# Optimization experiments

Hardware: AMD Instinct MI355X
Metric: run time of the kernel (lower is better)

Reference implementation:

```python
import jax, jax.numpy as jnp
import numpy as np

B, E, O, H = 4096, 1024, 16, 1024  # batch, embed_dim, num_ops, hidden_dim


def setup_inputs() -> dict:
    key = jax.random.key(0)
    k1, k2, k3, k4, k5, k6 = jax.random.split(key, 6)
    s1 = 1.0 / np.sqrt(E)
    s2 = 1.0 / np.sqrt(H)
    return {
        "x_aug": jax.random.normal(k1, (B, E), dtype=jnp.float32),
        "op_idx": jax.random.randint(k2, (B,), 0, O, dtype=jnp.int32),
        "W1": jax.random.normal(k3, (E, O, H), dtype=jnp.float32) * s1,  # DenseGeneral kernel: embed -> (ops, hidden)
        "b1": jnp.zeros((O, H), dtype=jnp.float32),
        "W2": jax.random.normal(k4, (H, O, H), dtype=jnp.float32) * s2,  # per-op second layer (diagonal of DenseGeneral)
        "b2": jnp.zeros((O, H), dtype=jnp.float32),
    }


def reference(x_aug, op_idx, W1, b1, W2, b2):
    # h1[b,o,h] = relu(sum_e x[b,e] W1[e,o,h] + b1[o,h])
    h1 = jax.nn.relu(jnp.einsum("be,eoh->boh", x_aug, W1) + b1)
    # h2[b,o,g] = relu(sum_h h1[b,o,h] W2[h,o,g] + b2[o,g])  (per-op MLP)
    h2 = jax.nn.relu(jnp.einsum("boh,hog->bog", h1, W2) + b2)
    # select the chosen operator's output per example
    idx = jnp.broadcast_to(op_idx[:, None, None], (x_aug.shape[0], 1, h2.shape[-1]))
    return jnp.take_along_axis(h2, idx, axis=1).squeeze(1)  # [B, H]
```

## Files before the change

### kernel.cpp

```cpp
#include <hip/hip_runtime.h>

#define Bn 4096
#define En 1024
#define On 16
#define Hn 1024
#define OHn (On * Hn)

#define BM 64
#define BN 128
#define BK 64

using floatx4 = __attribute__((ext_vector_type(4))) float;
using float4v = __attribute__((ext_vector_type(4))) float;
using bf16x8  = __attribute__((ext_vector_type(8))) __bf16;
using short8v = __attribute__((ext_vector_type(8))) short;

__device__ inline unsigned short f2bf(float f) {
    unsigned u = __builtin_bit_cast(unsigned, f);
    u += 0x7fffu + ((u >> 16) & 1u);
    return (unsigned short)(u >> 16);
}

__global__ void bucket_kernel(const int* __restrict__ op_idx,
                              int* __restrict__ sorted_idx,
                              int* __restrict__ offsets) {
    __shared__ int cnt[On], cur[On], off[On + 1];
    int tid = threadIdx.x;
    if (tid < On) { cnt[tid] = 0; cur[tid] = 0; }
    __syncthreads();
    for (int i = tid; i < Bn; i += blockDim.x) atomicAdd(&cnt[op_idx[i]], 1);
    __syncthreads();
    if (tid == 0) {
        int s = 0;
        for (int o = 0; o < On; ++o) { off[o] = s; s += cnt[o]; }
        off[On] = s;
    }
    __syncthreads();
    for (int i = tid; i < Bn; i += blockDim.x) {
        int o = op_idx[i];
        int p = off[o] + atomicAdd(&cur[o], 1);
        sorted_idx[p] = i;
    }
    if (tid <= On) offsets[tid] = off[tid];
}

__global__ __launch_bounds__(256) void gemm1_kernel(
    const float* __restrict__ x, const float* __restrict__ W1,
    const float* __restrict__ bias1, const int* __restrict__ sorted_idx,
    const int* __restrict__ offsets, unsigned short* __restrict__ h1) {
    int o = blockIdx.z;
    int off = offsets[o];
    int cnt = offsets[o + 1] - off;
    int m0 = blockIdx.y * BM;
    if (m0 >= cnt) return;
    int n0 = blockIdx.x * BN;

    __shared__ unsigned short As[8][BM][8];
    __shared__ unsigned short Bs[8][BN][8];

    int tid = threadIdx.x;

    int arow = tid & 63;
    int ag = tid >> 6;
    const float* aptr = nullptr;
    if (m0 + arow < cnt) aptr = x + (size_t)sorted_idx[off + m0 + arow] * En;

    int bn = tid & 127;
    int bg0 = (tid >> 7) * 4;
    const float* bptr = W1 + (size_t)o * Hn + n0 + bn;

    float a_pre[16] = {};
    float b_pre[32];

    floatx4 acc[2][4] = {};
    int lane = tid & 63;
    int wave = tid >> 6;
    int wm = (wave >> 1) * 32;
    int wn = (wave & 1) * 64;
    int l15 = lane & 15;
    int kg = lane >> 4;

#pragma unroll
    for (int i = 0; i < 2; ++i) {
        int k = (ag + 4 * i) * 8;
        if (aptr) {
            *(float4v*)&a_pre[i * 8]     = *(const float4v*)(aptr + k);
            *(float4v*)&a_pre[i * 8 + 4] = *(const float4v*)(aptr + k + 4);
        }
    }
#pragma unroll
    for (int g = 0; g < 4; ++g)
#pragma unroll
        for (int j = 0; j < 8; ++j)
            b_pre[g * 8 + j] = bptr[(size_t)((bg0 + g) * 8 + j) * OHn];

    for (int kt = 0; kt < En; kt += BK) {
#pragma unroll
        for (int i = 0; i < 2; ++i) {
            short8v v;
#pragma unroll
            for (int j = 0; j < 8; ++j) v[j] = (short)f2bf(a_pre[i * 8 + j]);
            *(short8v*)&As[ag + 4 * i][arow][0] = v;
        }
#pragma unroll
        for (int g = 0; g < 4; ++g) {
            short8v v;
#pragma unroll
            for (int j = 0; j < 8; ++j) v[j] = (short)f2bf(b_pre[g * 8 + j]);
            *(short8v*)&Bs[bg0 + g][bn][0] = v;
        }
        __syncthreads();

        int ktn = kt + BK;
        if (ktn < En) {
#pragma unroll
            for (int i = 0; i < 2; ++i) {
                int k = ktn + (ag + 4 * i) * 8;
                if (aptr) {
                    *(float4v*)&a_pre[i * 8]     = *(const float4v*)(aptr + k);
                    *(float4v*)&a_pre[i * 8 + 4] = *(const float4v*)(aptr + k + 4);
                }
            }
#pragma unroll
            for (int g = 0; g < 4; ++g)
#pragma unroll
                for (int j = 0; j < 8; ++j)
                    b_pre[g * 8 + j] = bptr[(size_t)(ktn + (bg0 + g) * 8 + j) * OHn];
        }

#pragma unroll
        for (int ks = 0; ks < 2; ++ks) {
            int g = ks * 4 + kg;
            bf16x8 af[2], bfr[4];
#pragma unroll
            for (int mt = 0; mt < 2; ++mt) af[mt] = *(const bf16x8*)&As[g][wm + mt * 16 + l15][0];
#pragma unroll
            for (int nt = 0; nt < 4; ++nt) bfr[nt] = *(const bf16x8*)&Bs[g][wn + nt * 16 + l15][0];
#pragma unroll
            for (int mt = 0; mt < 2; ++mt)
#pragma unroll
                for (int nt = 0; nt < 4; ++nt)
                    acc[mt][nt] = __builtin_amdgcn_mfma_f32_16x16x32_bf16(af[mt], bfr[nt], acc[mt][nt], 0, 0, 0);
        }
        __syncthreads();
    }

    int r4 = (lane >> 4) * 4;
#pragma unroll
    for (int nt = 0; nt < 4; ++nt) {
        int col = n0 + wn + nt * 16 + l15;
        float bv = bias1[o * Hn + col];
#pragma unroll
        for (int mt = 0; mt < 2; ++mt) {
#pragma unroll
            for (int r = 0; r < 4; ++r) {
                int row = m0 + wm + mt * 16 + r4 + r;
                if (row < cnt) {
                    float v = acc[mt][nt][r] + bv;
                    v = v > 0.f ? v : 0.f;
                    h1[(size_t)(off + row) * Hn + col] = f2bf(v);
                }
            }
        }
    }
}

__global__ __launch_bounds__(256) void gemm2_kernel(
    const unsigned short* __restrict__ h1, const float* __restrict__ W2,
    const float* __restrict__ bias2, const int* __restrict__ sorted_idx,
    const int* __restrict__ offsets, float* __restrict__ out) {
    int o = blockIdx.z;
    int off = offsets[o];
    int cnt = offsets[o + 1] - off;
    int m0 = blockIdx.y * BM;
    if (m0 >= cnt) return;
    int n0 = blockIdx.x * BN;

    __shared__ unsigned short As[8][BM][8];
    __shared__ unsigned short Bs[8][BN][8];

    int tid = threadIdx.x;

    int arow = tid & 63;
    int ag = tid >> 6;
    const unsigned short* aptr = nullptr;
    if (m0 + arow < cnt) aptr = h1 + (size_t)(off + m0 + arow) * Hn;

    int bn = tid & 127;
    int bg0 = (tid >> 7) * 4;
    const float* bptr = W2 + (size_t)o * Hn + n0 + bn;

    short8v a_pre[2] = {};
    float b_pre[32];

    floatx4 acc[2][4] = {};
    int lane = tid & 63;
    int wave = tid >> 6;
    int wm = (wave >> 1) * 32;
    int wn = (wave & 1) * 64;
    int l15 = lane & 15;
    int kg = lane >> 4;

#pragma unroll
    for (int i = 0; i < 2; ++i)
        if (aptr) a_pre[i] = *(const short8v*)(aptr + (ag + 4 * i) * 8);
#pragma unroll
    for (int g = 0; g < 4; ++g)
#pragma unroll
        for (int j = 0; j < 8; ++j)
            b_pre[g * 8 + j] = bptr[(size_t)((bg0 + g) * 8 + j) * OHn];

    for (int kt = 0; kt < Hn; kt += BK) {
#pragma unroll
        for (int i = 0; i < 2; ++i)
            *(short8v*)&As[ag + 4 * i][arow][0] = a_pre[i];
#pragma unroll
        for (int g = 0; g < 4; ++g) {
            short8v v;
#pragma unroll
            for (int j = 0; j < 8; ++j) v[j] = (short)f2bf(b_pre[g * 8 + j]);
            *(short8v*)&Bs[bg0 + g][bn][0] = v;
        }
        __syncthreads();

        int ktn = kt + BK;
        if (ktn < Hn) {
#pragma unroll
            for (int i = 0; i < 2; ++i)
                if (aptr) a_pre[i] = *(const short8v*)(aptr + ktn + (ag + 4 * i) * 8);
#pragma unroll
            for (int g = 0; g < 4; ++g)
#pragma unroll
                for (int j = 0; j < 8; ++j)
                    b_pre[g * 8 + j] = bptr[(size_t)(ktn + (bg0 + g) * 8 + j) * OHn];
        }

#pragma unroll
        for (int ks = 0; ks < 2; ++ks) {
            int g = ks * 4 + kg;
            bf16x8 af[2], bfr[4];
#pragma unroll
            for (int mt = 0; mt < 2; ++mt) af[mt] = *(const bf16x8*)&As[g][wm + mt * 16 + l15][0];
#pragma unroll
            for (int nt = 0; nt < 4; ++nt) bfr[nt] = *(const bf16x8*)&Bs[g][wn + nt * 16 + l15][0];
#pragma unroll
            for (int mt = 0; mt < 2; ++mt)
#pragma unroll
                for (int nt = 0; nt < 4; ++nt)
                    acc[mt][nt] = __builtin_amdgcn_mfma_f32_16x16x32_bf16(af[mt], bfr[nt], acc[mt][nt], 0, 0, 0);
        }
        __syncthreads();
    }

    int r4 = (lane >> 4) * 4;
    float bv[4];
#pragma unroll
    for (int nt = 0; nt < 4; ++nt) bv[nt] = bias2[o * Hn + n0 + wn + nt * 16 + l15];
#pragma unroll
    for (int mt = 0; mt < 2; ++mt) {
#pragma unroll
        for (int r = 0; r < 4; ++r) {
            int row = m0 + wm + mt * 16 + r4 + r;
            if (row < cnt) {
                int b = sorted_idx[off + row];
                float* orow = out + (size_t)b * Hn + n0 + wn + l15;
#pragma unroll
                for (int nt = 0; nt < 4; ++nt) {
                    float v = acc[mt][nt][r] + bv[nt];
                    orow[nt * 16] = v > 0.f ? v : 0.f;
                }
            }
        }
    }
}

extern "C" void kernel_launch(void* const* d_in, const int* in_sizes, int n_in,
                              void* d_out, int out_size, void* d_ws, size_t ws_size,
                              hipStream_t stream) {
    const float* x      = (const float*)d_in[0];
    const int*   op_idx = (const int*)d_in[1];
    const float* W1     = (const float*)d_in[2];
    const float* bias1  = (const float*)d_in[3];
    const float* W2     = (const float*)d_in[4];
    const float* bias2  = (const float*)d_in[5];
    float* out = (float*)d_out;

    char* ws = (char*)d_ws;
    int* offsets    = (int*)ws;
    int* sorted_idx = (int*)(ws + 256);
    unsigned short* h1 = (unsigned short*)(ws + 256 + 16384);

    hipLaunchKernelGGL(bucket_kernel, dim3(1), dim3(1024), 0, stream,
                       op_idx, sorted_idx, offsets);
    dim3 grid(Hn / BN, Bn / BM, On);
    hipLaunchKernelGGL(gemm1_kernel, grid, dim3(256), 0, stream,
                       x, W1, bias1, sorted_idx, offsets, h1);
    hipLaunchKernelGGL(gemm2_kernel, grid, dim3(256), 0, stream,
                       h1, W2, bias2, sorted_idx, offsets, out);
}
```

Baseline: 263.0 us.

## Pre-transpose weights and pre-gather x to bf16, load tiles via global_load_lds

```diff
diff --git a/kernel.cpp b/kernel.cpp
--- a/kernel.cpp
+++ b/kernel.cpp
@@ -4,7 +4,6 @@
 #define En 1024
 #define On 16
 #define Hn 1024
-#define OHn (On * Hn)
 
 #define BM 64
 #define BN 128
@@ -13,6 +12,7 @@
 using floatx4 = __attribute__((ext_vector_type(4))) float;
 using float4v = __attribute__((ext_vector_type(4))) float;
 using bf16x8  = __attribute__((ext_vector_type(8))) __bf16;
+using short4v = __attribute__((ext_vector_type(4))) short;
 using short8v = __attribute__((ext_vector_type(8))) short;
 
 __device__ inline unsigned short f2bf(float f) {
@@ -20,6 +20,10 @@
     u += 0x7fffu + ((u >> 16) & 1u);
     return (unsigned short)(u >> 16);
 }
+
+#define GLOAD16(gp, lp) __builtin_amdgcn_global_load_lds( \
+    (const __attribute__((address_space(1))) unsigned int*)(gp), \
+    (__attribute__((address_space(3))) unsigned int*)(lp), 16, 0, 0)
 
 __global__ void bucket_kernel(const int* __restrict__ op_idx,
                               int* __restrict__ sorted_idx,
@@ -44,13 +48,46 @@
     if (tid <= On) offsets[tid] = off[tid];
 }
 
+__global__ __launch_bounds__(256) void wtrans_kernel(const float* __restrict__ W,
+                                                     unsigned short* __restrict__ Wt) {
+    __shared__ float tile[64][65];
+    int o = blockIdx.z, e0 = blockIdx.y * 64, h0 = blockIdx.x * 64;
+    int t = threadIdx.x;
+    int er = t >> 4, c4 = (t & 15) * 4;
+#pragma unroll
+    for (int r = 0; r < 4; ++r) {
+        const float* p = W + ((size_t)(e0 + er + 16 * r) * On + o) * Hn + h0 + c4;
+        *(float4v*)&tile[er + 16 * r][c4] = *(const float4v*)p;
+    }
+    __syncthreads();
+    int hr = t >> 3, e8 = (t & 7) * 8;
+#pragma unroll
+    for (int r = 0; r < 2; ++r) {
+        short8v v;
+#pragma unroll
+        for (int j = 0; j < 8; ++j) v[j] = (short)f2bf(tile[e8 + j][hr + 32 * r]);
+        *(short8v*)(Wt + ((size_t)o * Hn + (h0 + hr + 32 * r)) * En + e0 + e8) = v;
+    }
+}
+
+__global__ __launch_bounds__(256) void xprep_kernel(const float* __restrict__ x,
+                                                    const int* __restrict__ sorted_idx,
+                                                    unsigned short* __restrict__ xs) {
+    int row = blockIdx.x;
+    int src = sorted_idx[row];
+    int t = threadIdx.x;
+    float4v f = *(const float4v*)(x + (size_t)src * En + t * 4);
+    short4v v = { (short)f2bf(f[0]), (short)f2bf(f[1]),
+                  (short)f2bf(f[2]), (short)f2bf(f[3]) };
+    *(short4v*)(xs + (size_t)row * En + t * 4) = v;
+}
+
 __global__ __launch_bounds__(256) void gemm1_kernel(
-    const float* __restrict__ x, const float* __restrict__ W1,
-    const float* __restrict__ bias1, const int* __restrict__ sorted_idx,
-    const int* __restrict__ offsets, unsigned short* __restrict__ h1) {
+    const unsigned short* __restrict__ xs, const unsigned short* __restrict__ Wt,
+    const float* __restrict__ bias1, const int* __restrict__ offsets,
+    unsigned short* __restrict__ h1) {
     int o = blockIdx.z;
-    int off = offsets[o];
-    int cnt = offsets[o + 1] - off;
+    int off = offsets[o], cnt = offsets[o + 1] - off;
     int m0 = blockIdx.y * BM;
     if (m0 >= cnt) return;
     int n0 = blockIdx.x * BN;
@@ -58,76 +95,28 @@
     __shared__ unsigned short As[8][BM][8];
     __shared__ unsigned short Bs[8][BN][8];
 
-    int tid = threadIdx.x;
-
-    int arow = tid & 63;
-    int ag = tid >> 6;
-    const float* aptr = nullptr;
-    if (m0 + arow < cnt) aptr = x + (size_t)sorted_idx[off + m0 + arow] * En;
-
-    int bn = tid & 127;
-    int bg0 = (tid >> 7) * 4;
-    const float* bptr = W1 + (size_t)o * Hn + n0 + bn;
-
-    float a_pre[16] = {};
-    float b_pre[32];
+    int tid = threadIdx.x, lane = tid & 63, wave = tid >> 6;
+    const unsigned short* Abase = xs + (size_t)(off + m0) * En;
+    const unsigned short* Bbase = Wt + ((size_t)o * Hn + n0) * En;
 
     floatx4 acc[2][4] = {};
-    int lane = tid & 63;
-    int wave = tid >> 6;
-    int wm = (wave >> 1) * 32;
-    int wn = (wave & 1) * 64;
-    int l15 = lane & 15;
-    int kg = lane >> 4;
-
-#pragma unroll
-    for (int i = 0; i < 2; ++i) {
-        int k = (ag + 4 * i) * 8;
-        if (aptr) {
-            *(float4v*)&a_pre[i * 8]     = *(const float4v*)(aptr + k);
-            *(float4v*)&a_pre[i * 8 + 4] = *(const float4v*)(aptr + k + 4);
-        }
-    }
-#pragma unroll
-    for (int g = 0; g < 4; ++g)
-#pragma unroll
-        for (int j = 0; j < 8; ++j)
-            b_pre[g * 8 + j] = bptr[(size_t)((bg0 + g) * 8 + j) * OHn];
+    int wm = (wave >> 1) * 32, wn = (wave & 1) * 64;
+    int l15 = lane & 15, kg = lane >> 4;
 
     for (int kt = 0; kt < En; kt += BK) {
 #pragma unroll
         for (int i = 0; i < 2; ++i) {
-            short8v v;
-#pragma unroll
-            for (int j = 0; j < 8; ++j) v[j] = (short)f2bf(a_pre[i * 8 + j]);
-            *(short8v*)&As[ag + 4 * i][arow][0] = v;
-        }
-#pragma unroll
-        for (int g = 0; g < 4; ++g) {
-            short8v v;
-#pragma unroll
-            for (int j = 0; j < 8; ++j) v[j] = (short)f2bf(b_pre[g * 8 + j]);
-            *(short8v*)&Bs[bg0 + g][bn][0] = v;
-        }
-        __syncthreads();
-
-        int ktn = kt + BK;
-        if (ktn < En) {
-#pragma unroll
-            for (int i = 0; i < 2; ++i) {
-                int k = ktn + (ag + 4 * i) * 8;
-                if (aptr) {
-                    *(float4v*)&a_pre[i * 8]     = *(const float4v*)(aptr + k);
-                    *(float4v*)&a_pre[i * 8 + 4] = *(const float4v*)(aptr + k + 4);
-                }
-            }
-#pragma unroll
-            for (int g = 0; g < 4; ++g)
-#pragma unroll
-                for (int j = 0; j < 8; ++j)
-                    b_pre[g * 8 + j] = bptr[(size_t)(ktn + (bg0 + g) * 8 + j) * OHn];
-        }
-
+            int g = wave * 2 + i;
+            GLOAD16(Abase + (size_t)lane * En + kt + g * 8, &As[g][0][0]);
+        }
+#pragma unroll
+        for (int i = 0; i < 4; ++i) {
+            int idx = wave * 4 + i;
+            int g = idx >> 1, half = idx & 1;
+            GLOAD16(Bbase + (size_t)(half * 64 + lane) * En + kt + g * 8,
+                    &Bs[g][half * 64][0]);
+        }
+        __syncthreads();
 #pragma unroll
         for (int ks = 0; ks < 2; ++ks) {
             int g = ks * 4 + kg;
@@ -166,12 +155,11 @@
 }
 
 __global__ __launch_bounds__(256) void gemm2_kernel(
-    const unsigned short* __restrict__ h1, const float* __restrict__ W2,
+    const unsigned short* __restrict__ h1, const unsigned short* __restrict__ Wt,
     const float* __restrict__ bias2, const int* __restrict__ sorted_idx,
     const int* __restrict__ offsets, float* __restrict__ out) {
     int o = blockIdx.z;
-    int off = offsets[o];
-    int cnt = offsets[o + 1] - off;
+    int off = offsets[o], cnt = offsets[o + 1] - off;
     int m0 = blockIdx.y * BM;
     if (m0 >= cnt) return;
     int n0 = blockIdx.x * BN;
@@ -179,62 +167,28 @@
     __shared__ unsigned short As[8][BM][8];
     __shared__ unsigned short Bs[8][BN][8];
 
-    int tid = threadIdx.x;
-
-    int arow = tid & 63;
-    int ag = tid >> 6;
-    const unsigned short* aptr = nullptr;
-    if (m0 + arow < cnt) aptr = h1 + (size_t)(off + m0 + arow) * Hn;
-
-    int bn = tid & 127;
-    int bg0 = (tid >> 7) * 4;
-    const float* bptr = W2 + (size_t)o * Hn + n0 + bn;
-
-    short8v a_pre[2] = {};
-    float b_pre[32];
+    int tid = threadIdx.x, lane = tid & 63, wave = tid >> 6;
+    const unsigned short* Abase = h1 + (size_t)(off + m0) * Hn;
+    const unsigned short* Bbase = Wt + ((size_t)o * Hn + n0) * Hn;
 
     floatx4 acc[2][4] = {};
-    int lane = tid & 63;
-    int wave = tid >> 6;
-    int wm = (wave >> 1) * 32;
-    int wn = (wave & 1) * 64;
-    int l15 = lane & 15;
-    int kg = lane >> 4;
-
-#pragma unroll
-    for (int i = 0; i < 2; ++i)
-        if (aptr) a_pre[i] = *(const short8v*)(aptr + (ag + 4 * i) * 8);
-#pragma unroll
-    for (int g = 0; g < 4; ++g)
-#pragma unroll
-        for (int j = 0; j < 8; ++j)
-            b_pre[g * 8 + j] = bptr[(size_t)((bg0 + g) * 8 + j) * OHn];
+    int wm = (wave >> 1) * 32, wn = (wave & 1) * 64;
+    int l15 = lane & 15, kg = lane >> 4;
 
     for (int kt = 0; kt < Hn; kt += BK) {
 #pragma unroll
-        for (int i = 0; i < 2; ++i)
-            *(short8v*)&As[ag + 4 * i][arow][0] = a_pre[i];
-#pragma unroll
-        for (int g = 0; g < 4; ++g) {
-            short8v v;
-#pragma unroll
-            for (int j = 0; j < 8; ++j) v[j] = (short)f2bf(b_pre[g * 8 + j]);
-            *(short8v*)&Bs[bg0 + g][bn][0] = v;
-        }
-        __syncthreads();
-
-        int ktn = kt + BK;
-        if (ktn < Hn) {
-#pragma unroll
-            for (int i = 0; i < 2; ++i)
-                if (aptr) a_pre[i] = *(const short8v*)(aptr + ktn + (ag + 4 * i) * 8);
-#pragma unroll
-            for (int g = 0; g < 4; ++g)
-#pragma unroll
-                for (int j = 0; j < 8; ++j)
-                    b_pre[g * 8 + j] = bptr[(size_t)(ktn + (bg0 + g) * 8 + j) * OHn];
-        }
-
+        for (int i = 0; i < 2; ++i) {
+            int g = wave * 2 + i;
+            GLOAD16(Abase + (size_t)lane * Hn + kt + g * 8, &As[g][0][0]);
+        }
+#pragma unroll
+        for (int i = 0; i < 4; ++i) {
+            int idx = wave * 4 + i;
+            int g = idx >> 1, half = idx & 1;
+            GLOAD16(Bbase + (size_t)(half * 64 + lane) * Hn + kt + g * 8,
+                    &Bs[g][half * 64][0]);
+        }
+        __syncthreads();
 #pragma unroll
         for (int ks = 0; ks < 2; ++ks) {
             int g = ks * 4 + kg;
@@ -287,14 +241,21 @@
 
     char* ws = (char*)d_ws;
     int* offsets    = (int*)ws;
-    int* sorted_idx = (int*)(ws + 256);
-    unsigned short* h1 = (unsigned short*)(ws + 256 + 16384);
-
+    int* sorted_idx = (int*)(ws + 1024);
+    unsigned short* xs = (unsigned short*)(ws + 65536);
+    unsigned short* h1 = (unsigned short*)(ws + 65536 + 8388608);
+    unsigned short* Wt = (unsigned short*)(ws + 65536 + 16777216);
+
+    dim3 tgrid(Hn / 64, En / 64, On);
+    hipLaunchKernelGGL(wtrans_kernel, tgrid, dim3(256), 0, stream, W1, Wt);
     hipLaunchKernelGGL(bucket_kernel, dim3(1), dim3(1024), 0, stream,
                        op_idx, sorted_idx, offsets);
+    hipLaunchKernelGGL(xprep_kernel, dim3(Bn), dim3(256), 0, stream,
+                       x, sorted_idx, xs);
     dim3 grid(Hn / BN, Bn / BM, On);
     hipLaunchKernelGGL(gemm1_kernel, grid, dim3(256), 0, stream,
-                       x, W1, bias1, sorted_idx, offsets, h1);
+                       xs, Wt, bias1, offsets, h1);
+    hipLaunchKernelGGL(wtrans_kernel, tgrid, dim3(256), 0, stream, W2, Wt);
     hipLaunchKernelGGL(gemm2_kernel, grid, dim3(256), 0, stream,
-                       h1, W2, bias2, sorted_idx, offsets, out);
-}
+                       h1, Wt, bias2, sorted_idx, offsets, out);
+}
```

After: 327.2 us. 1.24x slower.
